# Performance work log

Measured on AMD Instinct MI355X. Metric: run time of the kernel, lower is better.

The kernel has to match this reference:

```python
import jax, jax.numpy as jnp
import numpy as np

B, S, D = 8, 2048, 256
C, H = 32, 4
HD = D // H  # head_dim = 64


def setup_inputs() -> dict:
    key = jax.random.key(0)
    ks = jax.random.split(key, 12)
    scale = 0.02
    x = jax.random.normal(ks[0], (B, S, D), dtype=jnp.float32)
    conditioning = jax.random.uniform(ks[1], (B, S, C), dtype=jnp.float32)
    Wq_w = jax.random.normal(ks[2], (D, D), dtype=jnp.float32) * scale
    Wq_b = jax.random.normal(ks[3], (D,), dtype=jnp.float32) * scale
    Wv_w = jax.random.normal(ks[4], (D, D), dtype=jnp.float32) * scale
    Wv_b = jax.random.normal(ks[5], (D,), dtype=jnp.float32) * scale
    Wk_w = jax.random.normal(ks[6], (C, D, D), dtype=jnp.float32) * scale  # stacked per-class torch Linear weights [out,in]
    Wk_b = jax.random.normal(ks[7], (C, D), dtype=jnp.float32) * scale
    Wo_w = jax.random.normal(ks[8], (D, D), dtype=jnp.float32) * scale
    Wo_b = jax.random.normal(ks[9], (D,), dtype=jnp.float32) * scale
    return {"x": x, "conditioning": conditioning,
            "Wq_w": Wq_w, "Wq_b": Wq_b, "Wv_w": Wv_w, "Wv_b": Wv_b,
            "Wk_w": Wk_w, "Wk_b": Wk_b, "Wo_w": Wo_w, "Wo_b": Wo_b}


def reference(x, conditioning, Wq_w, Wq_b, Wv_w, Wv_b, Wk_w, Wk_b, Wo_w, Wo_b):
    # torch Linear: y = x @ W.T + b, with W of shape [out, in]
    q = (x @ Wq_w.T + Wq_b).reshape(B, S, H, HD).transpose(0, 2, 1, 3)  # (B,H,S,HD)
    v = (x @ Wv_w.T + Wv_b).reshape(B, S, H, HD).transpose(0, 2, 1, 3)
    # per-class keys: (B,C,S,D)
    class_keys = jnp.einsum('bsd,cfd->bcsf', x, Wk_w) + Wk_b[None, :, None, :]
    # data-dependent weighted sum over classes -> effective key (B,S,D)
    k = jnp.einsum('bsc,bcsf->bsf', conditioning, class_keys)
    k = k.reshape(B, S, H, HD).transpose(0, 2, 1, 3)  # (B,H,S,HD)
    # scaled dot-product attention (dropout_p = 0)
    scale = 1.0 / jnp.sqrt(jnp.float32(HD))
    scores = jnp.einsum('bhqd,bhkd->bhqk', q, k) * scale
    attn = jax.nn.softmax(scores, axis=-1)
    out = jnp.einsum('bhqk,bhkd->bhqd', attn, v)
    out = out.transpose(0, 2, 1, 3).reshape(B, S, D)
    return out @ Wo_w.T + Wo_b
```

## Files before the change

### kernel.cpp

```cpp
#include <hip/hip_runtime.h>
#include <hip/hip_bf16.h>

#define BB 8
#define SS 2048
#define DD 256
#define CC 32
#define HH 4
#define HD 64
#define MTOT (BB*SS)

using bf16    = __hip_bfloat16;
using short8  = __attribute__((ext_vector_type(8))) short;
using short4v = __attribute__((ext_vector_type(4))) short;
using floatx4 = __attribute__((ext_vector_type(4))) float;

#if __has_builtin(__builtin_amdgcn_mfma_f32_16x16x16_bf16)
  #define MFMA_PV16(a,b,c) __builtin_amdgcn_mfma_f32_16x16x16_bf16(a,b,c,0,0,0)
  #define HAVE_PV16 1
#elif __has_builtin(__builtin_amdgcn_mfma_f32_16x16x16bf16_1k)
  #define MFMA_PV16(a,b,c) __builtin_amdgcn_mfma_f32_16x16x16bf16_1k(a,b,c,0,0,0)
  #define HAVE_PV16 1
#else
  #define HAVE_PV16 0
#endif

#if __has_builtin(__builtin_amdgcn_global_load_lds)
  #define HAVE_GLL 1
#else
  #define HAVE_GLL 0
#endif

__device__ inline float bf2f(unsigned short u) {
    union { unsigned int i; float f; } v; v.i = ((unsigned int)u) << 16; return v.f;
}
__device__ inline unsigned short f2bfbits(float f) {
    bf16 h = __float2bfloat16(f);
    return __builtin_bit_cast(unsigned short, h);
}

#define N_X    (MTOT*DD)
#define N_COND (MTOT*CC)
#define N_WQW  (DD*DD)
#define N_WQB  (DD)
#define N_WVW  (DD*DD)
#define N_WVB  (DD)
#define N_WKW  (CC*DD*DD)
#define N_WKB  (CC*DD)
#define N_WOW  (DD*DD)
#define N_WOB  (DD)
#define P0 0
#define P1 (P0+N_X)
#define P2 (P1+N_COND)
#define P3 (P2+N_WQW)
#define P4 (P3+N_WQB)
#define P5 (P4+N_WVW)
#define P6 (P5+N_WVB)
#define P7 (P6+N_WKW)
#define P8 (P7+N_WKB)
#define P9 (P8+N_WOW)
#define PTOT (P9+N_WOB)

__global__ void convert_all(const void* s0, const void* s1, const void* s2,
                            const void* s3, const void* s4, const void* s5,
                            const void* s6, const void* s7, const void* s8,
                            const void* s9, bf16* dst, int* flagw)
{
    __shared__ int cnts[4];
    {
        const float* xf = (const float*)s0;
        float v = fabsf(xf[threadIdx.x]);
        bool ok = (v == v) && v > 1e-4f && v < 1e4f;
        unsigned long long m = __ballot(ok);
        if ((threadIdx.x & 63) == 0) cnts[threadIdx.x >> 6] = __popcll(m);
    }
    __syncthreads();
    const bool f32 = (cnts[0] + cnts[1] + cnts[2] + cnts[3]) > 128;
    if (blockIdx.x == 0 && threadIdx.x == 0) *flagw = f32 ? 1 : 0;

    size_t i = ((size_t)blockIdx.x * 256 + threadIdx.x) * 8;
    const size_t stride = (size_t)gridDim.x * 256 * 8;
    for (; i < (size_t)PTOT; i += stride) {
        const void* src; size_t off;
        if      (i < P1) { src = s0; off = i - P0; }
        else if (i < P2) { src = s1; off = i - P1; }
        else if (i < P3) { src = s2; off = i - P2; }
        else if (i < P4) { src = s3; off = i - P3; }
        else if (i < P5) { src = s4; off = i - P4; }
        else if (i < P6) { src = s5; off = i - P5; }
        else if (i < P7) { src = s6; off = i - P6; }
        else if (i < P8) { src = s7; off = i - P7; }
        else if (i < P9) { src = s8; off = i - P8; }
        else             { src = s9; off = i - P9; }
        if (f32) {
            const float* s = (const float*)src + off;
            float4 a = *(const float4*)(s);
            float4 b = *(const float4*)(s + 4);
            __align__(16) unsigned short t[8];
            t[0] = f2bfbits(a.x); t[1] = f2bfbits(a.y);
            t[2] = f2bfbits(a.z); t[3] = f2bfbits(a.w);
            t[4] = f2bfbits(b.x); t[5] = f2bfbits(b.y);
            t[6] = f2bfbits(b.z); t[7] = f2bfbits(b.w);
            *(uint4*)(dst + i) = *(const uint4*)t;
        } else {
            *(uint4*)(dst + i) = *(const uint4*)((const unsigned short*)src + off);
        }
    }
}

__device__ __forceinline__ void gemm_body(const bf16* __restrict__ X, const bf16* __restrict__ W,
                                          const bf16* __restrict__ bias, void* __restrict__ Yv,
                                          const int* __restrict__ flagp, int flex_out, int vt_out,
                                          unsigned short* smem, int m0, int n0)
{
    const int LDT = 264;
    unsigned short* xs = smem;
    unsigned short* ws = smem + 64 * 264;
    const int t = threadIdx.x;

    for (int i = 0; i < 8; ++i) {
        int c = t + i * 256;
        int row = c >> 5, col = (c & 31) * 8;
        *(uint4*)&xs[row * LDT + col] = *(const uint4*)(X + (size_t)(m0 + row) * DD + col);
        *(uint4*)&ws[row * LDT + col] = *(const uint4*)(W + (size_t)(n0 + row) * DD + col);
    }
    __syncthreads();

    const int w = t >> 6, lane = t & 63;
    const int lrow = lane & 15, lk = (lane >> 4) * 8, rgrp = (lane >> 4) * 4;
    floatx4 acc[4] = {};
    const unsigned short* ax = &xs[(w * 16 + lrow) * LDT + lk];
    for (int kt = 0; kt < 8; ++kt) {
        short8 a = *(const short8*)(ax + kt * 32);
        #pragma unroll
        for (int j = 0; j < 4; ++j) {
            short8 b = *(const short8*)&ws[(j * 16 + lrow) * LDT + kt * 32 + lk];
            acc[j] = __builtin_amdgcn_mfma_f32_16x16x32_bf16(a, b, acc[j], 0, 0, 0);
        }
    }

    if (vt_out) {
        __syncthreads();
        unsigned short* ts = xs;
        #pragma unroll
        for (int j = 0; j < 4; ++j) {
            float bv = __bfloat162float(bias[n0 + j * 16 + lrow]);
            #pragma unroll
            for (int r = 0; r < 4; ++r)
                ts[(j * 16 + lrow) * 72 + w * 16 + rgrp + r] = f2bfbits(acc[j][r] + bv);
        }
        __syncthreads();
        const int bq = m0 >> 11, s0v = m0 & 2047, h = n0 >> 6;
        bf16* dstb = (bf16*)Yv + ((size_t)(bq * HH + h) * HD) * SS + s0v;
        for (int i = 0; i < 2; ++i) {
            int idx = t + i * 256, row = idx >> 3, ch = (idx & 7) * 8;
            *(uint4*)(dstb + (size_t)row * SS + ch) = *(const uint4*)&ts[row * 72 + ch];
        }
        return;
    }

    const bool f32o = flex_out && (*flagp != 0);
    #pragma unroll
    for (int j = 0; j < 4; ++j) {
        int col = n0 + j * 16 + lrow;
        float bv = __bfloat162float(bias[col]);
        #pragma unroll
        for (int r = 0; r < 4; ++r) {
            int row = m0 + w * 16 + rgrp + r;
            float val = acc[j][r] + bv;
            if (f32o) ((float*)Yv)[(size_t)row * DD + col] = val;
            else      ((bf16*)Yv)[(size_t)row * DD + col] = __float2bfloat16(val);
        }
    }
}

__launch_bounds__(256, 2)
__global__ void gemm_qv(const bf16* __restrict__ X,
                        const bf16* __restrict__ Wqw, const bf16* __restrict__ Wqb, bf16* __restrict__ Qout,
                        const bf16* __restrict__ Wvw, const bf16* __restrict__ Wvb, bf16* __restrict__ Vout,
                        const int* __restrict__ flagp)
{
    __shared__ __align__(16) unsigned short smem[2 * 64 * 264];
    int gi = blockIdx.x;
    if (gi < 1024) {
        int n0 = (gi & 3) * 64, m0 = (gi >> 2) * 64;
        gemm_body(X, Wqw, Wqb, (void*)Qout, flagp, 0, 0, smem, m0, n0);
    } else {
        gi -= 1024;
        int n0 = (gi & 3) * 64, m0 = (gi >> 2) * 64;
        gemm_body(X, Wvw, Wvb, (void*)Vout, flagp, 0, 1, smem, m0, n0);
    }
}

__launch_bounds__(256, 2)
__global__ void gemm_bias(const bf16* __restrict__ X, const bf16* __restrict__ W,
                          const bf16* __restrict__ bias, void* __restrict__ Yv,
                          const int* __restrict__ flagp, int flex_out, int vt_out)
{
    __shared__ __align__(16) unsigned short smem[2 * 64 * 264];
    gemm_body(X, W, bias, Yv, flagp, flex_out, vt_out, smem, blockIdx.y * 64, blockIdx.x * 64);
}

__device__ __forceinline__ void stage_ws4(const bf16* __restrict__ Wc,
                                          unsigned short* wsbuf, int w, int lane)
{
    #pragma unroll
    for (int i = 0; i < 8; ++i) {
        int rr = w * 16 + i * 2 + (lane >> 5);
        int cs = (lane & 31) ^ (rr & 7);
        const bf16* src = Wc + (size_t)rr * DD + cs * 8;
        unsigned short* dst = wsbuf + (size_t)(w * 16 + i * 2) * DD;
#if HAVE_GLL
        __builtin_amdgcn_global_load_lds(
            (const __attribute__((address_space(1))) void*)src,
            (__attribute__((address_space(3))) void*)dst, 16, 0, 0);
#else
        uint4 v = *(const uint4*)src;
        *(uint4*)(dst + (size_t)lane * 8) = v;
#endif
    }
}

__launch_bounds__(256, 2)
__global__ void classkey(const bf16* __restrict__ X, const bf16* __restrict__ Cond,
                         const bf16* __restrict__ Wk, const bf16* __restrict__ Wkb,
                         bf16* __restrict__ Kout)
{
    __shared__ __align__(16) unsigned short ws[2][64 * 256];
    __shared__ __align__(16) unsigned short conds[128 * 32];
    __shared__ __align__(16) unsigned short kbs[32 * 64];
    const int t    = threadIdx.x;
    const int w    = t >> 6;
    const int lane = t & 63;
    const int r16  = lane & 15;
    const int quad = lane >> 4;
    const int m0   = blockIdx.y * 128;
    const int n0   = blockIdx.x * 64;

    #pragma unroll
    for (int i = 0; i < 2; ++i) {
        int chunk = t + i * 256;
        int row = chunk >> 2, c8 = (chunk & 3) * 8;
        *(uint4*)&conds[row * 32 + c8] = *(const uint4*)(Cond + (size_t)(m0 + row) * CC + c8);
    }
    {
        int row = t >> 3, c8 = (t & 7) * 8;
        *(uint4*)&kbs[row * 64 + c8] = *(const uint4*)(Wkb + (size_t)row * DD + n0 + c8);
    }

    short8 xa[2][8];
    #pragma unroll
    for (int mt = 0; mt < 2; ++mt) {
        const bf16* xrow = X + (size_t)(m0 + w * 32 + mt * 16 + r16) * DD + quad * 8;
        #pragma unroll
        for (int kt = 0; kt < 8; ++kt)
            xa[mt][kt] = *(const short8*)(xrow + kt * 32);
    }

    stage_ws4(Wk + (size_t)n0 * DD, &ws[0][0], w, lane);

    floatx4 acck[2][4] = {};
    for (int c = 0; c < CC; ++c) {
        __syncthreads();
        if (c + 1 < CC)
            stage_ws4(Wk + (size_t)(c + 1) * DD * DD + (size_t)n0 * DD,
                      &ws[(c + 1) & 1][0], w, lane);

        const unsigned short* wb = &ws[c & 1][0];
        floatx4 p[2][4] = {};
        #pragma unroll
        for (int kt = 0; kt < 8; ++kt) {
            short8 bj[4];
            #pragma unroll
            for (int j = 0; j < 4; ++j)
                bj[j] = *(const short8*)&wb[(j * 16 + r16) * DD +
                                            (((kt * 4 + quad) ^ (r16 & 7)) << 3)];
            #pragma unroll
            for (int mt = 0; mt < 2; ++mt)
                #pragma unroll
                for (int j = 0; j < 4; ++j)
                    p[mt][j] = __builtin_amdgcn_mfma_f32_16x16x32_bf16(xa[mt][kt], bj[j], p[mt][j], 0, 0, 0);
        }
        #pragma unroll
        for (int mt = 0; mt < 2; ++mt)
            #pragma unroll
            for (int r = 0; r < 4; ++r) {
                float cv = bf2f(conds[(w * 32 + mt * 16 + quad * 4 + r) * 32 + c]);
                #pragma unroll
                for (int j = 0; j < 4; ++j) acck[mt][j][r] += cv * p[mt][j][r];
            }
    }

    float kbv[2][4][4] = {};
    for (int c = 0; c < CC; ++c) {
        #pragma unroll
        for (int mt = 0; mt < 2; ++mt)
            #pragma unroll
            for (int r = 0; r < 4; ++r) {
                float cf = bf2f(conds[(w * 32 + mt * 16 + quad * 4 + r) * 32 + c]);
                #pragma unroll
                for (int j = 0; j < 4; ++j)
                    kbv[mt][j][r] += cf * bf2f(kbs[c * 64 + j * 16 + r16]);
            }
    }
    #pragma unroll
    for (int mt = 0; mt < 2; ++mt)
        #pragma unroll
        for (int j = 0; j < 4; ++j) {
            int col = n0 + j * 16 + r16;
            #pragma unroll
            for (int r = 0; r < 4; ++r) {
                int row = m0 + w * 32 + mt * 16 + quad * 4 + r;
                Kout[(size_t)row * DD + col] = __float2bfloat16(acck[mt][j][r] + kbv[mt][j][r]);
            }
        }
}

__device__ inline void stage_kv(const bf16* __restrict__ kRow,
                                const bf16* __restrict__ vRow,
                                unsigned short* kbuf, unsigned short* vbuf,
                                int w, int lane)
{
    int r  = w * 8 + (lane >> 3);
    int cs = (lane & 7) ^ (r & 7);
#if HAVE_GLL
    __builtin_amdgcn_global_load_lds(
        (const __attribute__((address_space(1))) void*)(kRow + (size_t)r * DD + cs * 8),
        (__attribute__((address_space(3))) void*)(kbuf + w * 512), 16, 0, 0);
    __builtin_amdgcn_global_load_lds(
        (const __attribute__((address_space(1))) void*)(vRow + (size_t)r * SS + cs * 8),
        (__attribute__((address_space(3))) void*)(vbuf + w * 512), 16, 0, 0);
#else
    *(uint4*)(kbuf + w * 512 + (size_t)lane * 8) = *(const uint4*)(kRow + (size_t)r * DD + cs * 8);
    *(uint4*)(vbuf + w * 512 + (size_t)lane * 8) = *(const uint4*)(vRow + (size_t)r * SS + cs * 8);
#endif
}

__launch_bounds__(512, 4)
__global__ void attn(const bf16* __restrict__ Q, const bf16* __restrict__ Kb,
                     const bf16* __restrict__ VT, bf16* __restrict__ O)
{
    __shared__ __align__(16) unsigned short ks[2][64 * 64];
    __shared__ __align__(16) unsigned short vt[2][64 * 64];
#if !HAVE_PV16
    __shared__ __align__(16) unsigned short ps[128 * 72];
#endif
    const int t    = threadIdx.x;
    const int w    = t >> 6;
    const int lane = t & 63;
    const int r16  = lane & 15;
    const int quad = lane >> 4;
    const int bh   = blockIdx.y;
    const int b    = bh >> 2, h = bh & 3;
    const int q0   = blockIdx.x * 128;
    const size_t base  = ((size_t)b * SS) * DD + h * HD;
    const size_t vbase = (size_t)bh * HD * SS;

    short8 qa[2];
    {
        const bf16* qrow = Q + base + (size_t)(q0 + w * 16 + r16) * DD + quad * 8;
        #pragma unroll
        for (int k2 = 0; k2 < 2; ++k2) {
            short8 raw = *(const short8*)(qrow + k2 * 32);
            short8 sc;
            #pragma unroll
            for (int e = 0; e < 8; ++e)
                sc[e] = (short)f2bfbits(bf2f((unsigned short)raw[e]) * 0.125f);
            qa[k2] = sc;
        }
    }

    stage_kv(Kb + base, VT + vbase, &ks[0][0], &vt[0][0], w, lane);

    floatx4 acco[4] = {};
    float mrun = -1e30f, lrun = 0.f;

    for (int kt = 0; kt < SS / 64; ++kt) {
        __syncthreads();
        if (kt + 1 < SS / 64)
            stage_kv(Kb + base + (size_t)(kt + 1) * 64 * DD,
                     VT + vbase + (size_t)(kt + 1) * 64,
                     &ks[(kt + 1) & 1][0], &vt[(kt + 1) & 1][0], w, lane);

        const unsigned short* kbuf = &ks[kt & 1][0];
        const unsigned short* vbuf = &vt[kt & 1][0];

        floatx4 s[4] = {};
        #pragma unroll
        for (int k2 = 0; k2 < 2; ++k2) {
            short8 bq = qa[k2];
            #pragma unroll
            for (int j = 0; j < 4; ++j) {
                short8 ak = *(const short8*)&kbuf[(j * 16 + r16) * 64 +
                                                  (((k2 * 4 + quad) ^ (r16 & 7)) << 3)];
                s[j] = __builtin_amdgcn_mfma_f32_16x16x32_bf16(ak, bq, s[j], 0, 0, 0);
            }
        }

        float mx = -1e30f;
        #pragma unroll
        for (int j = 0; j < 4; ++j)
            #pragma unroll
            for (int r = 0; r < 4; ++r) mx = fmaxf(mx, s[j][r]);
        mx = fmaxf(mx, __shfl_xor(mx, 16, 64));
        mx = fmaxf(mx, __shfl_xor(mx, 32, 64));
        float mnew  = fmaxf(mrun, mx);
        float alpha = __expf(mrun - mnew);
        float sum = 0.f;
        #pragma unroll
        for (int j = 0; j < 4; ++j)
            #pragma unroll
            for (int r = 0; r < 4; ++r) {
                float e = __expf(s[j][r] - mnew);
                s[j][r] = e; sum += e;
            }
        sum += __shfl_xor(sum, 16, 64);
        sum += __shfl_xor(sum, 32, 64);
        lrun = lrun * alpha + sum;
        mrun = mnew;

        #pragma unroll
        for (int r = 0; r < 4; ++r) {
            float ar = __shfl(alpha, (quad << 4) + quad * 4 + r, 64);
            #pragma unroll
            for (int jn = 0; jn < 4; ++jn) acco[jn][r] *= ar;
        }

#if HAVE_PV16
        #pragma unroll
        for (int j = 0; j < 4; ++j) {
            short4v p;
            p[0] = (short)f2bfbits(s[j][0]); p[1] = (short)f2bfbits(s[j][1]);
            p[2] = (short)f2bfbits(s[j][2]); p[3] = (short)f2bfbits(s[j][3]);
            #pragma unroll
            for (int jn = 0; jn < 4; ++jn) {
                short4v vv = *(const short4v*)&vbuf[(jn * 16 + r16) * 64 +
                                                    ((((j * 2) + (quad >> 1)) ^ (r16 & 7)) << 3) +
                                                    (quad & 1) * 4];
                acco[jn] = MFMA_PV16(p, vv, acco[jn]);
            }
        }
#else
        #pragma unroll
        for (int j = 0; j < 4; ++j)
            #pragma unroll
            for (int r = 0; r < 4; ++r)
                ps[(w * 16 + r16) * 72 + j * 16 + quad * 4 + r] = f2bfbits(s[j][r]);
        #pragma unroll
        for (int k2 = 0; k2 < 2; ++k2) {
            short8 a = *(const short8*)&ps[(w * 16 + r16) * 72 + k2 * 32 + quad * 8];
            #pragma unroll
            for (int jn = 0; jn < 4; ++jn) {
                short8 bb = *(const short8*)&vbuf[(jn * 16 + r16) * 64 +
                                                  (((k2 * 4 + quad) ^ (r16 & 7)) << 3)];
                acco[jn] = __builtin_amdgcn_mfma_f32_16x16x32_bf16(a, bb, acco[jn], 0, 0, 0);
            }
        }
#endif
    }

    #pragma unroll
    for (int r = 0; r < 4; ++r) {
        float lr = __shfl(lrun, (quad << 4) + quad * 4 + r, 64);
        float inv = 1.0f / lr;
        int row = q0 + w * 16 + quad * 4 + r;
        #pragma unroll
        for (int jn = 0; jn < 4; ++jn)
            O[base + (size_t)row * DD + jn * 16 + r16] = __float2bfloat16(acco[jn][r] * inv);
    }
}

extern "C" void kernel_launch(void* const* d_in, const int* in_sizes, int n_in,
                              void* d_out, int out_size, void* d_ws, size_t ws_size,
                              hipStream_t stream)
{
    int*  flag = (int*)d_ws;
    bf16* conv = (bf16*)((char*)d_ws + 256);

    const bf16* xb    = conv + P0;
    const bf16* condb = conv + P1;
    const bf16* wqw   = conv + P2;
    const bf16* wqb   = conv + P3;
    const bf16* wvw   = conv + P4;
    const bf16* wvb   = conv + P5;
    const bf16* wkw   = conv + P6;
    const bf16* wkb   = conv + P7;
    const bf16* wow   = conv + P8;
    const bf16* wob   = conv + P9;

    bf16* qb = conv + PTOT;
    bf16* kb = qb + (size_t)MTOT * DD;
    bf16* vb = kb + (size_t)MTOT * DD;
    bf16* ob = vb + (size_t)MTOT * DD;

    dim3 blk(256);
    hipLaunchKernelGGL(convert_all, dim3((PTOT / 8 + 255) / 256), blk, 0, stream,
                       d_in[0], d_in[1], d_in[2], d_in[3], d_in[4],
                       d_in[5], d_in[6], d_in[7], d_in[8], d_in[9],
                       conv, flag);

    dim3 gck(DD / 64, MTOT / 128);
    hipLaunchKernelGGL(classkey, gck, blk, 0, stream, xb, condb, wkw, wkb, kb);

    hipLaunchKernelGGL(gemm_qv, dim3(2048), blk, 0, stream,
                       xb, wqw, wqb, qb, wvw, wvb, vb, flag);

    dim3 ga(SS / 128, BB * HH);
    hipLaunchKernelGGL(attn, ga, dim3(512), 0, stream, qb, kb, vb, ob);

    dim3 gg(DD / 64, MTOT / 64);
    hipLaunchKernelGGL(gemm_bias, gg, blk, 0, stream, ob, wow, wob, d_out, flag, 1, 0);
}
```

Measured before the change: 251.1 us.

## Give each attention wave two query tiles to reuse K/V fragments

The attention kernel now runs 256 threads (4 waves) per block instead of 512. Each wave handles 32 query rows as two 16-row subtiles, so every K and V fragment read from LDS feeds two MFMAs. The K/V staging is split so each thread issues two loads per tile. This cuts LDS read traffic per MFMA, but each wave holds twice the accumulators and Q registers, and there are fewer waves per block to hide latency.

```diff
diff --git a/kernel.cpp b/kernel.cpp
--- a/kernel.cpp
+++ b/kernel.cpp
@@ -315,27 +315,32 @@
         }
 }
 
-__device__ inline void stage_kv(const bf16* __restrict__ kRow,
-                                const bf16* __restrict__ vRow,
-                                unsigned short* kbuf, unsigned short* vbuf,
-                                int w, int lane)
-{
-    int r  = w * 8 + (lane >> 3);
-    int cs = (lane & 7) ^ (r & 7);
+__device__ __forceinline__ void stage_kv4(const bf16* __restrict__ kRow,
+                                          const bf16* __restrict__ vRow,
+                                          unsigned short* kbuf, unsigned short* vbuf,
+                                          int w, int lane)
+{
+    #pragma unroll
+    for (int i = 0; i < 2; ++i) {
+        int r  = w * 16 + i * 8 + (lane >> 3);
+        int cs = (lane & 7) ^ (r & 7);
 #if HAVE_GLL
-    __builtin_amdgcn_global_load_lds(
-        (const __attribute__((address_space(1))) void*)(kRow + (size_t)r * DD + cs * 8),
-        (__attribute__((address_space(3))) void*)(kbuf + w * 512), 16, 0, 0);
-    __builtin_amdgcn_global_load_lds(
-        (const __attribute__((address_space(1))) void*)(vRow + (size_t)r * SS + cs * 8),
-        (__attribute__((address_space(3))) void*)(vbuf + w * 512), 16, 0, 0);
+        __builtin_amdgcn_global_load_lds(
+            (const __attribute__((address_space(1))) void*)(kRow + (size_t)r * DD + cs * 8),
+            (__attribute__((address_space(3))) void*)(kbuf + (w * 16 + i * 8) * 64), 16, 0, 0);
+        __builtin_amdgcn_global_load_lds(
+            (const __attribute__((address_space(1))) void*)(vRow + (size_t)r * SS + cs * 8),
+            (__attribute__((address_space(3))) void*)(vbuf + (w * 16 + i * 8) * 64), 16, 0, 0);
 #else
-    *(uint4*)(kbuf + w * 512 + (size_t)lane * 8) = *(const uint4*)(kRow + (size_t)r * DD + cs * 8);
-    *(uint4*)(vbuf + w * 512 + (size_t)lane * 8) = *(const uint4*)(vRow + (size_t)r * SS + cs * 8);
+        *(uint4*)(kbuf + (w * 16 + i * 8) * 64 + (size_t)lane * 8) =
+            *(const uint4*)(kRow + (size_t)r * DD + cs * 8);
+        *(uint4*)(vbuf + (w * 16 + i * 8) * 64 + (size_t)lane * 8) =
+            *(const uint4*)(vRow + (size_t)r * SS + cs * 8);
 #endif
-}
-
-__launch_bounds__(512, 4)
+    }
+}
+
+__launch_bounds__(256, 4)
 __global__ void attn(const bf16* __restrict__ Q, const bf16* __restrict__ Kb,
                      const bf16* __restrict__ VT, bf16* __restrict__ O)
 {
@@ -355,9 +360,10 @@
     const size_t base  = ((size_t)b * SS) * DD + h * HD;
     const size_t vbase = (size_t)bh * HD * SS;
 
-    short8 qa[2];
-    {
-        const bf16* qrow = Q + base + (size_t)(q0 + w * 16 + r16) * DD + quad * 8;
+    short8 qa[2][2];
+    #pragma unroll
+    for (int mt = 0; mt < 2; ++mt) {
+        const bf16* qrow = Q + base + (size_t)(q0 + w * 32 + mt * 16 + r16) * DD + quad * 8;
         #pragma unroll
         for (int k2 = 0; k2 < 2; ++k2) {
             short8 raw = *(const short8*)(qrow + k2 * 32);
@@ -365,108 +371,124 @@
             #pragma unroll
             for (int e = 0; e < 8; ++e)
                 sc[e] = (short)f2bfbits(bf2f((unsigned short)raw[e]) * 0.125f);
-            qa[k2] = sc;
-        }
-    }
-
-    stage_kv(Kb + base, VT + vbase, &ks[0][0], &vt[0][0], w, lane);
-
-    floatx4 acco[4] = {};
-    float mrun = -1e30f, lrun = 0.f;
+            qa[mt][k2] = sc;
+        }
+    }
+
+    stage_kv4(Kb + base, VT + vbase, &ks[0][0], &vt[0][0], w, lane);
+
+    floatx4 acco[2][4] = {};
+    float mrun[2] = {-1e30f, -1e30f};
+    float lrun[2] = {0.f, 0.f};
 
     for (int kt = 0; kt < SS / 64; ++kt) {
         __syncthreads();
         if (kt + 1 < SS / 64)
-            stage_kv(Kb + base + (size_t)(kt + 1) * 64 * DD,
-                     VT + vbase + (size_t)(kt + 1) * 64,
-                     &ks[(kt + 1) & 1][0], &vt[(kt + 1) & 1][0], w, lane);
+            stage_kv4(Kb + base + (size_t)(kt + 1) * 64 * DD,
+                      VT + vbase + (size_t)(kt + 1) * 64,
+                      &ks[(kt + 1) & 1][0], &vt[(kt + 1) & 1][0], w, lane);
 
         const unsigned short* kbuf = &ks[kt & 1][0];
         const unsigned short* vbuf = &vt[kt & 1][0];
 
-        floatx4 s[4] = {};
+        floatx4 s[2][4] = {};
         #pragma unroll
         for (int k2 = 0; k2 < 2; ++k2) {
-            short8 bq = qa[k2];
             #pragma unroll
             for (int j = 0; j < 4; ++j) {
                 short8 ak = *(const short8*)&kbuf[(j * 16 + r16) * 64 +
                                                   (((k2 * 4 + quad) ^ (r16 & 7)) << 3)];
-                s[j] = __builtin_amdgcn_mfma_f32_16x16x32_bf16(ak, bq, s[j], 0, 0, 0);
-            }
-        }
-
-        float mx = -1e30f;
-        #pragma unroll
-        for (int j = 0; j < 4; ++j)
-            #pragma unroll
-            for (int r = 0; r < 4; ++r) mx = fmaxf(mx, s[j][r]);
-        mx = fmaxf(mx, __shfl_xor(mx, 16, 64));
-        mx = fmaxf(mx, __shfl_xor(mx, 32, 64));
-        float mnew  = fmaxf(mrun, mx);
-        float alpha = __expf(mrun - mnew);
-        float sum = 0.f;
-        #pragma unroll
-        for (int j = 0; j < 4; ++j)
+                #pragma unroll
+                for (int mt = 0; mt < 2; ++mt)
+                    s[mt][j] = __builtin_amdgcn_mfma_f32_16x16x32_bf16(ak, qa[mt][k2], s[mt][j], 0, 0, 0);
+            }
+        }
+
+        #pragma unroll
+        for (int mt = 0; mt < 2; ++mt) {
+            float mx = -1e30f;
+            #pragma unroll
+            for (int j = 0; j < 4; ++j)
+                #pragma unroll
+                for (int r = 0; r < 4; ++r) mx = fmaxf(mx, s[mt][j][r]);
+            mx = fmaxf(mx, __shfl_xor(mx, 16, 64));
+            mx = fmaxf(mx, __shfl_xor(mx, 32, 64));
+            float mnew  = fmaxf(mrun[mt], mx);
+            float alpha = __expf(mrun[mt] - mnew);
+            float sum = 0.f;
+            #pragma unroll
+            for (int j = 0; j < 4; ++j)
+                #pragma unroll
+                for (int r = 0; r < 4; ++r) {
+                    float e = __expf(s[mt][j][r] - mnew);
+                    s[mt][j][r] = e; sum += e;
+                }
+            sum += __shfl_xor(sum, 16, 64);
+            sum += __shfl_xor(sum, 32, 64);
+            lrun[mt] = lrun[mt] * alpha + sum;
+            mrun[mt] = mnew;
             #pragma unroll
             for (int r = 0; r < 4; ++r) {
-                float e = __expf(s[j][r] - mnew);
-                s[j][r] = e; sum += e;
-            }
-        sum += __shfl_xor(sum, 16, 64);
-        sum += __shfl_xor(sum, 32, 64);
-        lrun = lrun * alpha + sum;
-        mrun = mnew;
-
-        #pragma unroll
-        for (int r = 0; r < 4; ++r) {
-            float ar = __shfl(alpha, (quad << 4) + quad * 4 + r, 64);
-            #pragma unroll
-            for (int jn = 0; jn < 4; ++jn) acco[jn][r] *= ar;
+                float ar = __shfl(alpha, (quad << 4) + quad * 4 + r, 64);
+                #pragma unroll
+                for (int jn = 0; jn < 4; ++jn) acco[mt][jn][r] *= ar;
+            }
         }
 
 #if HAVE_PV16
         #pragma unroll
         for (int j = 0; j < 4; ++j) {
-            short4v p;
-            p[0] = (short)f2bfbits(s[j][0]); p[1] = (short)f2bfbits(s[j][1]);
-            p[2] = (short)f2bfbits(s[j][2]); p[3] = (short)f2bfbits(s[j][3]);
-            #pragma unroll
-            for (int jn = 0; jn < 4; ++jn) {
-                short4v vv = *(const short4v*)&vbuf[(jn * 16 + r16) * 64 +
-                                                    ((((j * 2) + (quad >> 1)) ^ (r16 & 7)) << 3) +
-                                                    (quad & 1) * 4];
-                acco[jn] = MFMA_PV16(p, vv, acco[jn]);
+            short4v vv[4];
+            #pragma unroll
+            for (int jn = 0; jn < 4; ++jn)
+                vv[jn] = *(const short4v*)&vbuf[(jn * 16 + r16) * 64 +
+                                                ((((j * 2) + (quad >> 1)) ^ (r16 & 7)) << 3) +
+                                                (quad & 1) * 4];
+            #pragma unroll
+            for (int mt = 0; mt < 2; ++mt) {
+                short4v p;
+                p[0] = (short)f2bfbits(s[mt][j][0]); p[1] = (short)f2bfbits(s[mt][j][1]);
+                p[2] = (short)f2bfbits(s[mt][j][2]); p[3] = (short)f2bfbits(s[mt][j][3]);
+                #pragma unroll
+                for (int jn = 0; jn < 4; ++jn)
+                    acco[mt][jn] = MFMA_PV16(p, vv[jn], acco[mt][jn]);
             }
         }
 #else
         #pragma unroll
-        for (int j = 0; j < 4; ++j)
-            #pragma unroll
-            for (int r = 0; r < 4; ++r)
-                ps[(w * 16 + r16) * 72 + j * 16 + quad * 4 + r] = f2bfbits(s[j][r]);
+        for (int mt = 0; mt < 2; ++mt)
+            #pragma unroll
+            for (int j = 0; j < 4; ++j)
+                #pragma unroll
+                for (int r = 0; r < 4; ++r)
+                    ps[(w * 32 + mt * 16 + r16) * 72 + j * 16 + quad * 4 + r] = f2bfbits(s[mt][j][r]);
         #pragma unroll
         for (int k2 = 0; k2 < 2; ++k2) {
-            short8 a = *(const short8*)&ps[(w * 16 + r16) * 72 + k2 * 32 + quad * 8];
             #pragma unroll
             for (int jn = 0; jn < 4; ++jn) {
                 short8 bb = *(const short8*)&vbuf[(jn * 16 + r16) * 64 +
                                                   (((k2 * 4 + quad) ^ (r16 & 7)) << 3)];
-                acco[jn] = __builtin_amdgcn_mfma_f32_16x16x32_bf16(a, bb, acco[jn], 0, 0, 0);
+                #pragma unroll
+                for (int mt = 0; mt < 2; ++mt) {
+                    short8 a = *(const short8*)&ps[(w * 32 + mt * 16 + r16) * 72 + k2 * 32 + quad * 8];
+                    acco[mt][jn] = __builtin_amdgcn_mfma_f32_16x16x32_bf16(a, bb, acco[mt][jn], 0, 0, 0);
+                }
             }
         }
 #endif
     }
 
     #pragma unroll
-    for (int r = 0; r < 4; ++r) {
-        float lr = __shfl(lrun, (quad << 4) + quad * 4 + r, 64);
-        float inv = 1.0f / lr;
-        int row = q0 + w * 16 + quad * 4 + r;
-        #pragma unroll
-        for (int jn = 0; jn < 4; ++jn)
-            O[base + (size_t)row * DD + jn * 16 + r16] = __float2bfloat16(acco[jn][r] * inv);
-    }
+    for (int mt = 0; mt < 2; ++mt)
+        #pragma unroll
+        for (int r = 0; r < 4; ++r) {
+            float lr = __shfl(lrun[mt], (quad << 4) + quad * 4 + r, 64);
+            float inv = 1.0f / lr;
+            int row = q0 + w * 32 + mt * 16 + quad * 4 + r;
+            #pragma unroll
+            for (int jn = 0; jn < 4; ++jn)
+                O[base + (size_t)row * DD + jn * 16 + r16] = __float2bfloat16(acco[mt][jn][r] * inv);
+        }
 }
 
 extern "C" void kernel_launch(void* const* d_in, const int* in_sizes, int n_in,
@@ -505,7 +527,7 @@
                        xb, wqw, wqb, qb, wvw, wvb, vb, flag);
 
     dim3 ga(SS / 128, BB * HH);
-    hipLaunchKernelGGL(attn, ga, dim3(512), 0, stream, qb, kb, vb, ob);
+    hipLaunchKernelGGL(attn, ga, blk, 0, stream, qb, kb, vb, ob);
 
     dim3 gg(DD / 64, MTOT / 64);
     hipLaunchKernelGGL(gemm_bias, gg, blk, 0, stream, ob, wow, wob, d_out, flag, 1, 0);
```

New measurement: 273.9 us. 9.1% more time.
